# Kernel optimization log

Hardware: AMD Instinct MI355X
Metric: run time of the kernel (lower is better)

## Reference

```python
import jax, jax.numpy as jnp
import numpy as np

B, D = 1024, 512   # batch, feature dim (input_shape[1])
K, NC = 256, 1     # output_dim, num_centers (mask broadcast requires NC==1)


def setup_inputs() -> dict:
    key = jax.random.key(0)
    k1, k2, k3 = jax.random.split(key, 3)
    x = jax.random.normal(k1, (B, D), dtype=jnp.float32)
    # w_mean params (keras Constant init in the original; randomized for a nontrivial test)
    means = jax.random.normal(k2, (K, NC, D), dtype=jnp.float32) * 0.1
    # w_rho params (keras 'uniform' init: U[-0.05, 0.05]); sigma = softplus(rho)
    rho = jax.random.uniform(k3, (K, NC, D), minval=-0.05, maxval=0.05, dtype=jnp.float32)
    return {"x": x, "means": means, "rho": rho}


def reference(x, means, rho):
    # sigma = log(1 + exp(rho)), computed in build()
    sigma = jnp.log1p(jnp.exp(rho))                      # (K, NC, D)
    # squared difference, broadcast over all classes/centers at once
    d2 = (x[None, None, :, :] - means[:, :, None, :]) ** 2   # (K, NC, B, D)
    sig2 = sigma * sigma                                  # (K, NC, D)
    # logits[idx*NC + c][b] = sum_d d2/2 * sigma^2
    logits = jnp.sum(d2 * (0.5 * sig2)[:, :, None, :], axis=-1)   # (K, NC, B)
    # gaussian activation: exp(-sum_d d2 / (2 sigma^2))
    G = jnp.exp(-jnp.sum(d2 / (2.0 * sig2)[:, :, None, :], axis=-1))  # (K, NC, B)
    # P = (max_c G * (NC+1) - sum_c G) / NC
    P = (jnp.max(G, axis=1) * (NC + 1) - jnp.sum(G, axis=1)) / NC     # (K, B)
    probs = P.T                                           # (B, K)
    # stack order in TF: idx-major, c-minor -> (B, K*NC)
    logits_bk = jnp.transpose(logits, (2, 0, 1))          # (B, K, NC)
    mask = (probs >= 0.0).astype(logits_bk.dtype)         # (B, K)
    out = logits_bk * mask[:, :, None]                    # broadcast over NC (==1)
    return out.reshape(B, K * NC)
```

## Files before the change

### kernel.cpp

```cpp
#include <hip/hip_runtime.h>
#include <hip/hip_bf16.h>


#define BB 1024
#define DD 512
#define DP 1024
#define KK 256

typedef __attribute__((ext_vector_type(8))) short bf16x8;
typedef __attribute__((ext_vector_type(4))) float f32x4;
typedef __attribute__((ext_vector_type(4))) unsigned short us4;

static __device__ inline unsigned short f2bf(float f) {
    __hip_bfloat16 h = __float2bfloat16(f);
    return *reinterpret_cast<unsigned short*>(&h);
}

__global__ __launch_bounds__(256) void prep_x_kernel(const float* __restrict__ x,
                                                     unsigned short* __restrict__ Xp) {
    const int i = blockIdx.x * 256 + threadIdx.x;
    const int b = i >> 7;
    const int d4 = (i & 127) * 4;
    const float4 xv = *(const float4*)&x[b * DD + d4];
    us4 sq, ln;
    sq.x = f2bf(xv.x * xv.x); sq.y = f2bf(xv.y * xv.y);
    sq.z = f2bf(xv.z * xv.z); sq.w = f2bf(xv.w * xv.w);
    ln.x = f2bf(xv.x); ln.y = f2bf(xv.y); ln.z = f2bf(xv.z); ln.w = f2bf(xv.w);
    *(us4*)&Xp[b * DP + d4]      = sq;
    *(us4*)&Xp[b * DP + DD + d4] = ln;
}

__global__ __launch_bounds__(256) void prep_w_kernel(const float* __restrict__ means,
                                                     const float* __restrict__ rho,
                                                     unsigned short* __restrict__ Wp,
                                                     float* __restrict__ c) {
    const int k = blockIdx.x;
    const int t = threadIdx.x;
    __shared__ float red[256];
    float csum = 0.f;
#pragma unroll
    for (int d = t; d < DD; d += 256) {
        const float r  = rho[k * DD + d];
        const float m  = means[k * DD + d];
        const float sp = log1pf(expf(r));
        const float wv = 0.5f * sp * sp;
        Wp[k * DP + d]      = f2bf(wv);
        Wp[k * DP + DD + d] = f2bf(-2.0f * wv * m);
        csum += wv * m * m;
    }
    red[t] = csum;
    __syncthreads();
    for (int off = 128; off > 0; off >>= 1) {
        if (t < off) red[t] += red[t + off];
        __syncthreads();
    }
    if (t == 0) c[k] = red[0];
}

__global__ __launch_bounds__(256) void gemm_kernel(const unsigned short* __restrict__ Xp,
                                                   const unsigned short* __restrict__ Wp,
                                                   const float* __restrict__ c,
                                                   float* __restrict__ out) {
    const int lane = threadIdx.x & 63;
    const int wave = threadIdx.x >> 6;
    const int tile = blockIdx.x * 4 + wave;
    const int kb = tile & 15;
    const int bb = tile >> 4;
    const int k0 = kb * 16;
    const int b0 = bb * 16;

    const int rc   = lane & 15;
    const int quad = lane >> 4;

    const unsigned short* aRow = Xp + (b0 + rc) * DP + quad * 8;
    const unsigned short* bRow = Wp + (k0 + rc) * DP + quad * 8;

    f32x4 acc = {0.f, 0.f, 0.f, 0.f};
#pragma unroll 4
    for (int dk = 0; dk < DP; dk += 32) {
        const bf16x8 a = *(const bf16x8*)(aRow + dk);
        const bf16x8 b = *(const bf16x8*)(bRow + dk);
        acc = __builtin_amdgcn_mfma_f32_16x16x32_bf16(a, b, acc, 0, 0, 0);
    }

    const int col = rc;
    const int row0 = quad * 4;
    const float cv = c[k0 + col];
#pragma unroll
    for (int r = 0; r < 4; r++) {
        out[(b0 + row0 + r) * KK + (k0 + col)] = acc[r] + cv;
    }
}

extern "C" void kernel_launch(void* const* d_in, const int* in_sizes, int n_in,
                              void* d_out, int out_size, void* d_ws, size_t ws_size,
                              hipStream_t stream) {
    const float* x     = (const float*)d_in[0];
    const float* means = (const float*)d_in[1];
    const float* rho   = (const float*)d_in[2];
    float* out = (float*)d_out;

    unsigned short* Xp = (unsigned short*)d_ws;
    unsigned short* Wp = Xp + (size_t)BB * DP;
    float* c = (float*)(Wp + (size_t)KK * DP);

    prep_x_kernel<<<(BB * DD / 4) / 256, 256, 0, stream>>>(x, Xp);
    prep_w_kernel<<<KK, 256, 0, stream>>>(means, rho, Wp, c);
    gemm_kernel<<<256, 256, 0, stream>>>(Xp, Wp, c, out);
}
```

Measured before the change: 71.25 us.

## Fuse x/w preprocessing into the MFMA GEMM with LDS-staged chunked prefetch

Replaces the three-kernel pipeline (prep x, prep w, GEMM) with one kernel. Each block converts its x tile and its weight slice to bf16 in LDS, chunk by chunk along D, and prefetches the next chunk into registers while the MFMAs run. The per-class constant is reduced inside the block. This removes two launches and the workspace round trip, at the cost of recomputing softplus and the x squares in every block that shares the same data.

```diff
diff --git a/kernel.cpp b/kernel.cpp
--- a/kernel.cpp
+++ b/kernel.cpp
@@ -4,8 +4,10 @@
 
 #define BB 1024
 #define DD 512
-#define DP 1024
 #define KK 256
+#define DC 64
+#define NCHUNK (DD / DC)
+#define XSTR 72
 
 typedef __attribute__((ext_vector_type(8))) short bf16x8;
 typedef __attribute__((ext_vector_type(4))) float f32x4;
@@ -16,79 +18,112 @@
     return *reinterpret_cast<unsigned short*>(&h);
 }
 
-__global__ __launch_bounds__(256) void prep_x_kernel(const float* __restrict__ x,
-                                                     unsigned short* __restrict__ Xp) {
-    const int i = blockIdx.x * 256 + threadIdx.x;
-    const int b = i >> 7;
-    const int d4 = (i & 127) * 4;
-    const float4 xv = *(const float4*)&x[b * DD + d4];
-    us4 sq, ln;
-    sq.x = f2bf(xv.x * xv.x); sq.y = f2bf(xv.y * xv.y);
-    sq.z = f2bf(xv.z * xv.z); sq.w = f2bf(xv.w * xv.w);
-    ln.x = f2bf(xv.x); ln.y = f2bf(xv.y); ln.z = f2bf(xv.z); ln.w = f2bf(xv.w);
-    *(us4*)&Xp[b * DP + d4]      = sq;
-    *(us4*)&Xp[b * DP + DD + d4] = ln;
-}
+__global__ __launch_bounds__(256) void fused_kernel(const float* __restrict__ x,
+                                                    const float* __restrict__ means,
+                                                    const float* __restrict__ rho,
+                                                    float* __restrict__ out) {
+    __shared__ unsigned short xsq[64][XSTR];
+    __shared__ unsigned short xln[64][XSTR];
+    __shared__ unsigned short wT[16][XSTR];
+    __shared__ unsigned short aT[16][XSTR];
+    __shared__ float red[256];
+    __shared__ float csh[16];
 
-__global__ __launch_bounds__(256) void prep_w_kernel(const float* __restrict__ means,
-                                                     const float* __restrict__ rho,
-                                                     unsigned short* __restrict__ Wp,
-                                                     float* __restrict__ c) {
-    const int k = blockIdx.x;
-    const int t = threadIdx.x;
-    __shared__ float red[256];
+    const int t    = threadIdx.x;
+    const int kb   = blockIdx.x & 15;
+    const int bb   = blockIdx.x >> 4;
+    const int k0   = kb * 16;
+    const int b0   = bb * 64;
+    const int lane = t & 63;
+    const int wave = t >> 6;
+    const int col  = lane & 15;
+    const int quad = lane >> 4;
+
+    const int wk  = t >> 4;
+    const int wc4 = t & 15;
+
+    float4 xr[4];
+    float4 mr, rr;
+
+#pragma unroll
+    for (int j = 0; j < 4; j++) {
+        const int idx = j * 256 + t;
+        const int row = idx >> 4, c4 = idx & 15;
+        xr[j] = *(const float4*)&x[(b0 + row) * DD + c4 * 4];
+    }
+    mr = *(const float4*)&means[(k0 + wk) * DD + wc4 * 4];
+    rr = *(const float4*)&rho  [(k0 + wk) * DD + wc4 * 4];
+
+    f32x4 acc = {0.f, 0.f, 0.f, 0.f};
     float csum = 0.f;
+
+    for (int ic = 0; ic < NCHUNK; ic++) {
 #pragma unroll
-    for (int d = t; d < DD; d += 256) {
-        const float r  = rho[k * DD + d];
-        const float m  = means[k * DD + d];
-        const float sp = log1pf(expf(r));
-        const float wv = 0.5f * sp * sp;
-        Wp[k * DP + d]      = f2bf(wv);
-        Wp[k * DP + DD + d] = f2bf(-2.0f * wv * m);
-        csum += wv * m * m;
+        for (int j = 0; j < 4; j++) {
+            const int idx = j * 256 + t;
+            const int row = idx >> 4, c4 = idx & 15;
+            const float4 v = xr[j];
+            us4 sq, ln;
+            sq.x = f2bf(v.x * v.x); sq.y = f2bf(v.y * v.y);
+            sq.z = f2bf(v.z * v.z); sq.w = f2bf(v.w * v.w);
+            ln.x = f2bf(v.x); ln.y = f2bf(v.y); ln.z = f2bf(v.z); ln.w = f2bf(v.w);
+            *(us4*)&xsq[row][c4 * 4] = sq;
+            *(us4*)&xln[row][c4 * 4] = ln;
+        }
+        {
+            us4 wq, aq;
+            float sp, wv;
+            sp = log1pf(expf(rr.x)); wv = 0.5f * sp * sp;
+            wq.x = f2bf(wv); aq.x = f2bf(-2.f * wv * mr.x); csum += wv * mr.x * mr.x;
+            sp = log1pf(expf(rr.y)); wv = 0.5f * sp * sp;
+            wq.y = f2bf(wv); aq.y = f2bf(-2.f * wv * mr.y); csum += wv * mr.y * mr.y;
+            sp = log1pf(expf(rr.z)); wv = 0.5f * sp * sp;
+            wq.z = f2bf(wv); aq.z = f2bf(-2.f * wv * mr.z); csum += wv * mr.z * mr.z;
+            sp = log1pf(expf(rr.w)); wv = 0.5f * sp * sp;
+            wq.w = f2bf(wv); aq.w = f2bf(-2.f * wv * mr.w); csum += wv * mr.w * mr.w;
+            *(us4*)&wT[wk][wc4 * 4] = wq;
+            *(us4*)&aT[wk][wc4 * 4] = aq;
+        }
+        __syncthreads();
+
+        if (ic + 1 < NCHUNK) {
+            const int d0 = (ic + 1) * DC;
+#pragma unroll
+            for (int j = 0; j < 4; j++) {
+                const int idx = j * 256 + t;
+                const int row = idx >> 4, c4 = idx & 15;
+                xr[j] = *(const float4*)&x[(b0 + row) * DD + d0 + c4 * 4];
+            }
+            mr = *(const float4*)&means[(k0 + wk) * DD + d0 + wc4 * 4];
+            rr = *(const float4*)&rho  [(k0 + wk) * DD + d0 + wc4 * 4];
+        }
+
+#pragma unroll
+        for (int dk = 0; dk < DC; dk += 32) {
+            const bf16x8 a_sq = *(const bf16x8*)&xsq[wave * 16 + col][dk + quad * 8];
+            const bf16x8 a_ln = *(const bf16x8*)&xln[wave * 16 + col][dk + quad * 8];
+            const bf16x8 b_w  = *(const bf16x8*)&wT[col][dk + quad * 8];
+            const bf16x8 b_a  = *(const bf16x8*)&aT[col][dk + quad * 8];
+            acc = __builtin_amdgcn_mfma_f32_16x16x32_bf16(a_sq, b_w, acc, 0, 0, 0);
+            acc = __builtin_amdgcn_mfma_f32_16x16x32_bf16(a_ln, b_a, acc, 0, 0, 0);
+        }
+        __syncthreads();
     }
+
     red[t] = csum;
     __syncthreads();
-    for (int off = 128; off > 0; off >>= 1) {
-        if (t < off) red[t] += red[t + off];
-        __syncthreads();
+    if (t < 16) {
+        float s = 0.f;
+#pragma unroll
+        for (int j = 0; j < 16; j++) s += red[t * 16 + j];
+        csh[t] = s;
     }
-    if (t == 0) c[k] = red[0];
-}
+    __syncthreads();
 
-__global__ __launch_bounds__(256) void gemm_kernel(const unsigned short* __restrict__ Xp,
-                                                   const unsigned short* __restrict__ Wp,
-                                                   const float* __restrict__ c,
-                                                   float* __restrict__ out) {
-    const int lane = threadIdx.x & 63;
-    const int wave = threadIdx.x >> 6;
-    const int tile = blockIdx.x * 4 + wave;
-    const int kb = tile & 15;
-    const int bb = tile >> 4;
-    const int k0 = kb * 16;
-    const int b0 = bb * 16;
-
-    const int rc   = lane & 15;
-    const int quad = lane >> 4;
-
-    const unsigned short* aRow = Xp + (b0 + rc) * DP + quad * 8;
-    const unsigned short* bRow = Wp + (k0 + rc) * DP + quad * 8;
-
-    f32x4 acc = {0.f, 0.f, 0.f, 0.f};
-#pragma unroll 4
-    for (int dk = 0; dk < DP; dk += 32) {
-        const bf16x8 a = *(const bf16x8*)(aRow + dk);
-        const bf16x8 b = *(const bf16x8*)(bRow + dk);
-        acc = __builtin_amdgcn_mfma_f32_16x16x32_bf16(a, b, acc, 0, 0, 0);
-    }
-
-    const int col = rc;
-    const int row0 = quad * 4;
-    const float cv = c[k0 + col];
+    const float cv = csh[col];
 #pragma unroll
     for (int r = 0; r < 4; r++) {
-        out[(b0 + row0 + r) * KK + (k0 + col)] = acc[r] + cv;
+        out[(b0 + wave * 16 + quad * 4 + r) * KK + (k0 + col)] = acc[r] + cv;
     }
 }
 
@@ -100,11 +135,5 @@
     const float* rho   = (const float*)d_in[2];
     float* out = (float*)d_out;
 
-    unsigned short* Xp = (unsigned short*)d_ws;
-    unsigned short* Wp = Xp + (size_t)BB * DP;
-    float* c = (float*)(Wp + (size_t)KK * DP);
-
-    prep_x_kernel<<<(BB * DD / 4) / 256, 256, 0, stream>>>(x, Xp);
-    prep_w_kernel<<<KK, 256, 0, stream>>>(means, rho, Wp, c);
-    gemm_kernel<<<256, 256, 0, stream>>>(Xp, Wp, c, out);
+    fused_kernel<<<256, 256, 0, stream>>>(x, means, rho, out);
 }
```

Measured after the change: 73.42 us. 1.03x slower.
